# Kernel optimization log

Hardware: AMD Instinct MI355X
Metric: run time of the kernel (lower is better)

## Reference

```python
import jax, jax.numpy as jnp
import numpy as np

DELTA = 6.0      # 3 / (1 - alpha), alpha = 0.5
ETA = 1.0
MS_ITER = 3
D_FEAT = 256
N_PTS = 8192
X_SCALE = 0.06   # keeps ||x||^2 ~ 0.9 so exp(DELTA * X^T X) is well-conditioned


def setup_inputs() -> dict:
    key = jax.random.key(0)
    X = jax.random.normal(key, (D_FEAT, N_PTS), dtype=jnp.float32) * X_SCALE
    return {"X": X}


def _mean_shift_once(X):
    # X: [d, N]
    S = jnp.einsum('dn,dm->nm', X, X)          # X^T X, [N, N]
    K = jnp.exp(DELTA * S)                     # Gaussian-like affinity, [N, N]
    colsum = jnp.sum(K, axis=0)                # d = K^T @ ones  -> column sums, [N]
    # X @ P with P = (1-eta) I + eta K D_inv; D_inv = diag(1/colsum).
    # X @ K @ D_inv == (X @ K) / colsum (per-column scaling) -- no diag/eye materialized.
    XK = X @ K                                 # [d, N]
    return (1.0 - ETA) * X + ETA * (XK / colsum[None, :])


def reference(X):
    outs = []
    cur = X
    for _ in range(MS_ITER):
        cur = _mean_shift_once(cur)
        outs.append(cur)
    return tuple(outs)
```

## Files before the change

### kernel.cpp

```cpp
#include <hip/hip_runtime.h>
#include <hip/hip_bf16.h>
#include <stdint.h>

#define DFEAT 256
#define NPTS  8192

typedef __attribute__((ext_vector_type(8)))  short bf16x8;
typedef __attribute__((ext_vector_type(16))) float f32x16;
typedef __attribute__((ext_vector_type(4)))  int   int4v;
typedef __attribute__((ext_vector_type(4)))  float f32x4;

#define AS1 __attribute__((address_space(1)))
#define AS3 __attribute__((address_space(3)))

__device__ inline void dma16(const void* g, void* l) {
  __builtin_amdgcn_global_load_lds((const AS1 uint32_t*)g, (AS3 uint32_t*)l, 16, 0, 0);
}

__device__ inline uint16_t f2bf(float f) {
  union { float f; uint32_t u; } v; v.f = f;
  return (uint16_t)((v.u + 0x7FFFu + ((v.u >> 16) & 1u)) >> 16);
}


__global__ __launch_bounds__(256, 2) void ms_fused(
    const uint16_t* __restrict__ xaf,
    const uint16_t* __restrict__ xbf,
    float* __restrict__ num,
    float* __restrict__ cs)
{
  __shared__ __attribute__((aligned(16))) uint16_t XT[2][16384];
  __shared__ __attribute__((aligned(16))) uint16_t Ps[2][4096];

  const int tid  = threadIdx.x;
  const int w    = tid >> 6;
  const int lane = tid & 63;
  const int l31  = lane & 31;
  const int g    = lane >> 5;
  const int bid  = blockIdx.x;
  const int mt   = (bid & 1) | ((bid >> 3) << 1);
  const int q    = (bid >> 1) & 3;
  const int m0   = mt * 64;
  const int a_sub = w >> 1;
  const int b_sub = w & 1;

  const char* xafc = (const char*)xaf;
  const char* xbfc = (const char*)xbf;
  char*       XTc  = (char*)XT;
  char*       Psc  = (char*)Ps;

  bf16x8 Bm[16];
  {
    const char* bp = xafc + (size_t)(m0 / 32 + b_sub) * 16384 + g * 512 + l31 * 16;
    #pragma unroll
    for (int ks = 0; ks < 16; ++ks)
      Bm[ks] = __builtin_bit_cast(bf16x8, *(const int4v*)(bp + ks * 1024));
  }

  f32x16 accO[2][2];
  #pragma unroll
  for (int i = 0; i < 2; ++i)
    #pragma unroll
    for (int j = 0; j < 2; ++j)
      #pragma unroll
      for (int r = 0; r < 16; ++r) accO[i][j][r] = 0.0f;
  float csacc = 0.0f;

  const int mloc = 32 * b_sub + l31;
  const int l7   = l31 & 7;
  const int j0   = q * 32;

  {
    const char* src = xafc + (size_t)j0 * 32768;
    #pragma unroll
    for (int r = 0; r < 8; ++r)
      dma16(src + tid * 16 + r * 4096, XTc + tid * 16 + r * 4096);
  }
  __syncthreads();

  bf16x8 XfE[2][4], XfO[2][4];

#define MS_BODY(T_, CUR_, XF_LD, XF_USE, DO_PV)                               \
  {                                                                           \
    const int jt_ = j0 + (T_);                                                \
    char*       psW_ = Psc + (CUR_) * 8192;                                   \
    const char* psR_ = Psc + ((CUR_) ^ 1) * 8192;                             \
                         \
    if ((T_) < 31) {                                                          \
      const char* src_ = xafc + (size_t)(jt_ + 1) * 32768;                    \
      _Pragma("unroll")                                                       \
      for (int r = 0; r < 8; ++r)                                             \
        dma16(src_ + tid * 16 + r * 4096,                                     \
              XTc + ((CUR_) ^ 1) * 32768 + tid * 16 + r * 4096);              \
    }                                                                         \
                                \
    {                                                                         \
      const int n0_ = jt_ * 64;                                               \
      _Pragma("unroll")                                                       \
      for (int t2 = 0; t2 < 2; ++t2) {                                        \
        const char* xp_ = xbfc + (size_t)(2 * w + t2) * 524288 +              \
                          (size_t)(n0_ >> 3) * 512 + g * 512 + l31 * 16;      \
        _Pragma("unroll")                                                     \
        for (int ks = 0; ks < 4; ++ks)                                        \
          XF_LD[t2][ks] =                                                     \
              __builtin_bit_cast(bf16x8, *(const int4v*)(xp_ + ks * 1024));   \
      }                                                                       \
    }                                                                         \
              \
    __builtin_amdgcn_sched_barrier(0x38F);                                    \
              \
    f32x16 s;                                                                 \
    _Pragma("unroll")                                                         \
    for (int r = 0; r < 16; ++r) s[r] = 0.0f;                                 \
    {                                                                         \
      const char* ap_ = XTc + (CUR_) * 32768 + a_sub * 16384 + g * 512 +      \
                        l31 * 16;                                             \
      _Pragma("unroll")                                                       \
      for (int ks = 0; ks < 16; ++ks) {                                       \
        bf16x8 A = __builtin_bit_cast(bf16x8,                                 \
                                      *(const int4v*)(ap_ + ks * 1024));      \
        s = __builtin_amdgcn_mfma_f32_32x32x16_bf16(A, Bm[ks], s, 0, 0, 0);   \
      }                                                                       \
    }                                                                         \
                                \
    if (DO_PV) {                                                              \
      _Pragma("unroll")                                                       \
      for (int ks = 0; ks < 4; ++ks) {                                        \
        bf16x8 Bp[2];                                                         \
        _Pragma("unroll")                                                     \
        for (int mm = 0; mm < 2; ++mm) {                                      \
          int mrow = 32 * mm + l31;                                           \
          int p = (2 * ks + g) ^ l7;                                          \
          Bp[mm] = __builtin_bit_cast(bf16x8,                                 \
              *(const int4v*)(psR_ + mrow * 128 + p * 16));                   \
        }                                                                     \
        _Pragma("unroll")                                                     \
        for (int t2 = 0; t2 < 2; ++t2) {                                      \
          accO[t2][0] = __builtin_amdgcn_mfma_f32_32x32x16_bf16(              \
              XF_USE[t2][ks], Bp[0], accO[t2][0], 0, 0, 0);                   \
          accO[t2][1] = __builtin_amdgcn_mfma_f32_32x32x16_bf16(              \
              XF_USE[t2][ks], Bp[1], accO[t2][1], 0, 0, 0);                   \
        }                                                                     \
      }                                                                       \
    }                                                                         \
                        \
    _Pragma("unroll")                                                         \
    for (int k = 0; k < 4; ++k) {                                             \
      float e0 = __expf(6.0f * s[4 * k + 0]);                                 \
      float e1 = __expf(6.0f * s[4 * k + 1]);                                 \
      float e2 = __expf(6.0f * s[4 * k + 2]);                                 \
      float e3 = __expf(6.0f * s[4 * k + 3]);                                 \
      csacc += (e0 + e1) + (e2 + e3);                                         \
      uint32_t lo, hi;                                                        \
      asm("v_cvt_pk_bf16_f32 %0, %1, %2" : "=v"(lo) : "v"(e0), "v"(e1));      \
      asm("v_cvt_pk_bf16_f32 %0, %1, %2" : "=v"(hi) : "v"(e2), "v"(e3));      \
      int p = (4 * a_sub + k) ^ (mloc & 7);                                   \
      *(uint64_t*)(psW_ + mloc * 128 + p * 16 + 8 * g) =                      \
          ((uint64_t)hi << 32) | lo;                                          \
    }                                                                         \
          \
    asm volatile("s_waitcnt vmcnt(8) lgkmcnt(0)" ::: "memory");               \
    __builtin_amdgcn_s_barrier();                                             \
  }

  MS_BODY(0, 0, XfE, XfO, false)
  for (int tp = 0; tp < 15; ++tp) {
    const int tb = 2 * tp;
    MS_BODY(tb + 1, 1, XfO, XfE, true)
    MS_BODY(tb + 2, 0, XfE, XfO, true)
  }
  MS_BODY(31, 1, XfO, XfE, true)
#undef MS_BODY

  {
    const char* psR = Psc + 8192;
    #pragma unroll
    for (int ks = 0; ks < 4; ++ks) {
      bf16x8 Bp[2];
      #pragma unroll
      for (int mm = 0; mm < 2; ++mm) {
        int mrow = 32 * mm + l31;
        int p = (2 * ks + g) ^ l7;
        Bp[mm] = __builtin_bit_cast(bf16x8,
            *(const int4v*)(psR + mrow * 128 + p * 16));
      }
      #pragma unroll
      for (int t2 = 0; t2 < 2; ++t2) {
        accO[t2][0] = __builtin_amdgcn_mfma_f32_32x32x16_bf16(XfO[t2][ks], Bp[0], accO[t2][0], 0,0,0);
        accO[t2][1] = __builtin_amdgcn_mfma_f32_32x32x16_bf16(XfO[t2][ks], Bp[1], accO[t2][1], 0,0,0);
      }
    }
  }

  csacc += __shfl_xor(csacc, 32, 64);
  if (g == 0) atomicAdd(&cs[m0 + mloc], csacc);
  #pragma unroll
  for (int t2 = 0; t2 < 2; ++t2)
    #pragma unroll
    for (int mm = 0; mm < 2; ++mm)
      #pragma unroll
      for (int r = 0; r < 16; ++r) {
        int drow = 32 * (2 * w + t2) + (r & 3) + 8 * (r >> 2) + 4 * g;
        int mg   = m0 + 32 * mm + l31;
        atomicAdd(&num[(size_t)drow * NPTS + mg], accO[t2][mm][r]);
      }
}

__global__ __launch_bounds__(256) void ms_combine(
    const float* __restrict__ src, const float* __restrict__ csr,
    float* __restrict__ csz, float* __restrict__ yout,
    float* __restrict__ numz,
    uint16_t* __restrict__ xaf, uint16_t* __restrict__ xbf,
    const int mode)
{
  __shared__ uint16_t T[64][66];
  const int tid = threadIdx.x;
  const int n0 = blockIdx.x * 64;
  const int d0 = blockIdx.y * 64;

  #pragma unroll
  for (int i = 0; i < 4; ++i) {
    int e  = tid + i * 256;
    int dl = e >> 4, nq = e & 15;
    size_t idx = (size_t)(d0 + dl) * NPTS + (n0 + nq * 4);
    f32x4 v = *(const f32x4*)(src + idx);
    if (mode) {
      f32x4 c = *(const f32x4*)(csr + n0 + nq * 4);
      v /= c;
      *(f32x4*)(yout + idx) = v;
      f32x4 z = {0.f, 0.f, 0.f, 0.f};
      *(f32x4*)(numz + idx) = z;
    }
    #pragma unroll
    for (int k = 0; k < 4; ++k) T[dl][nq * 4 + k] = f2bf(v[k]);
  }
  if (mode && blockIdx.y == 0 && tid < 64) csz[n0 + tid] = 0.0f;
  __syncthreads();

  char* xafc = (char*)xaf;
  char* xbfc = (char*)xbf;
  #pragma unroll
  for (int i = 0; i < 2; ++i) {
    int c  = tid + i * 256;
    int nb = c >> 8, s2 = (c >> 5) & 7, ln = c & 31;
    union { uint32_t u[4]; int4v v; } pk;
    #pragma unroll
    for (int k = 0; k < 4; ++k) {
      uint32_t lo = T[s2 * 8 + 2 * k][nb * 32 + ln];
      uint32_t hi = T[s2 * 8 + 2 * k + 1][nb * 32 + ln];
      pk.u[k] = lo | (hi << 16);
    }
    *(int4v*)(xafc + (size_t)(n0 / 32 + nb) * 16384 +
              (size_t)(d0 / 8 + s2) * 512 + ln * 16) = pk.v;
  }
  #pragma unroll
  for (int i = 0; i < 2; ++i) {
    int c  = tid + i * 256;
    int db = c >> 8, uu = (c >> 5) & 7, ln = c & 31;
    const uint16_t* tr = &T[db * 32 + ln][uu * 8];
    union { uint32_t u[4]; int4v v; } pk;
    #pragma unroll
    for (int k = 0; k < 4; ++k)
      pk.u[k] = (uint32_t)tr[2 * k] | ((uint32_t)tr[2 * k + 1] << 16);
    *(int4v*)(xbfc + (size_t)(d0 / 32 + db) * 524288 +
              (size_t)(n0 / 8 + uu) * 512 + ln * 16) = pk.v;
  }
}

extern "C" void kernel_launch(void* const* d_in, const int* in_sizes, int n_in,
                              void* d_out, int out_size, void* d_ws, size_t ws_size,
                              hipStream_t stream)
{
  (void)in_sizes; (void)n_in; (void)out_size; (void)ws_size;
  const float* X = (const float*)d_in[0];
  float* out = (float*)d_out;
  char* ws = (char*)d_ws;
  uint16_t* xaf = (uint16_t*)(ws);
  uint16_t* xbf = (uint16_t*)(ws + (4u << 20));
  float*    num = (float*)   (ws + (8u << 20));
  float*    cs0 = (float*)   (ws + (16u << 20));
  float*    cs1 = (float*)   (ws + (16u << 20) + 32768);

  hipMemsetAsync(ws + (8u << 20), 0, (8u << 20) + 65536, stream);

  dim3 cgrid(NPTS / 64, DFEAT / 64);
  ms_combine<<<cgrid, 256, 0, stream>>>(X, nullptr, nullptr, nullptr, nullptr,
                                        xaf, xbf, 0);
  for (int it = 0; it < 3; ++it) {
    float* csA = (it & 1) ? cs1 : cs0;
    float* csB = (it & 1) ? cs0 : cs1;
    ms_fused<<<512, 256, 0, stream>>>(xaf, xbf, num, csA);
    ms_combine<<<cgrid, 256, 0, stream>>>(num, csA, csB,
                                          out + (size_t)it * DFEAT * NPTS,
                                          num, xaf, xbf, 1);
  }
}
```

Measured before the change: 337.5 us.

## Replace global atomic accumulation with per-split partial buffers reduced in combine

Instead of atomically adding partial numerator and column-sum results into shared global buffers, each of the four q-splits writes its own partial slab with plain stores, and the combine kernel sums the four slabs (and eight column-sum partials) before normalizing. This removes the atomic traffic and the memset/zeroing of accumulators. In exchange it costs more workspace and four times the numerator read traffic in the combine kernel.

```diff
diff --git a/kernel.cpp b/kernel.cpp
--- a/kernel.cpp
+++ b/kernel.cpp
@@ -26,8 +26,8 @@
 __global__ __launch_bounds__(256, 2) void ms_fused(
     const uint16_t* __restrict__ xaf,
     const uint16_t* __restrict__ xbf,
-    float* __restrict__ num,
-    float* __restrict__ cs)
+    float* __restrict__ nump,
+    float* __restrict__ csp)
 {
   __shared__ __attribute__((aligned(16))) uint16_t XT[2][16384];
   __shared__ __attribute__((aligned(16))) uint16_t Ps[2][4096];
@@ -193,7 +193,8 @@
   }
 
   csacc += __shfl_xor(csacc, 32, 64);
-  if (g == 0) atomicAdd(&cs[m0 + mloc], csacc);
+  if (g == 0) csp[(size_t)(2 * q + a_sub) * NPTS + m0 + mloc] = csacc;
+  float* np = nump + (size_t)q * (DFEAT * (size_t)NPTS);
   #pragma unroll
   for (int t2 = 0; t2 < 2; ++t2)
     #pragma unroll
@@ -202,14 +203,13 @@
       for (int r = 0; r < 16; ++r) {
         int drow = 32 * (2 * w + t2) + (r & 3) + 8 * (r >> 2) + 4 * g;
         int mg   = m0 + 32 * mm + l31;
-        atomicAdd(&num[(size_t)drow * NPTS + mg], accO[t2][mm][r]);
+        np[(size_t)drow * NPTS + mg] = accO[t2][mm][r];
       }
 }
 
 __global__ __launch_bounds__(256) void ms_combine(
-    const float* __restrict__ src, const float* __restrict__ csr,
-    float* __restrict__ csz, float* __restrict__ yout,
-    float* __restrict__ numz,
+    const float* __restrict__ src, const float* __restrict__ csp,
+    float* __restrict__ yout,
     uint16_t* __restrict__ xaf, uint16_t* __restrict__ xbf,
     const int mode)
 {
@@ -218,6 +218,17 @@
   const int n0 = blockIdx.x * 64;
   const int d0 = blockIdx.y * 64;
 
+  f32x4 rinv;
+  if (mode) {
+    const int nq = tid & 15;
+    f32x4 c = *(const f32x4*)(csp + n0 + nq * 4);
+    #pragma unroll
+    for (int s2 = 1; s2 < 8; ++s2)
+      c += *(const f32x4*)(csp + (size_t)s2 * NPTS + n0 + nq * 4);
+    rinv[0] = 1.0f / c[0]; rinv[1] = 1.0f / c[1];
+    rinv[2] = 1.0f / c[2]; rinv[3] = 1.0f / c[3];
+  }
+
   #pragma unroll
   for (int i = 0; i < 4; ++i) {
     int e  = tid + i * 256;
@@ -225,16 +236,15 @@
     size_t idx = (size_t)(d0 + dl) * NPTS + (n0 + nq * 4);
     f32x4 v = *(const f32x4*)(src + idx);
     if (mode) {
-      f32x4 c = *(const f32x4*)(csr + n0 + nq * 4);
-      v /= c;
+      v += *(const f32x4*)(src + idx + (size_t)1 * DFEAT * NPTS);
+      v += *(const f32x4*)(src + idx + (size_t)2 * DFEAT * NPTS);
+      v += *(const f32x4*)(src + idx + (size_t)3 * DFEAT * NPTS);
+      v *= rinv;
       *(f32x4*)(yout + idx) = v;
-      f32x4 z = {0.f, 0.f, 0.f, 0.f};
-      *(f32x4*)(numz + idx) = z;
     }
     #pragma unroll
     for (int k = 0; k < 4; ++k) T[dl][nq * 4 + k] = f2bf(v[k]);
   }
-  if (mode && blockIdx.y == 0 && tid < 64) csz[n0 + tid] = 0.0f;
   __syncthreads();
 
   char* xafc = (char*)xaf;
@@ -275,23 +285,18 @@
   const float* X = (const float*)d_in[0];
   float* out = (float*)d_out;
   char* ws = (char*)d_ws;
-  uint16_t* xaf = (uint16_t*)(ws);
-  uint16_t* xbf = (uint16_t*)(ws + (4u << 20));
-  float*    num = (float*)   (ws + (8u << 20));
-  float*    cs0 = (float*)   (ws + (16u << 20));
-  float*    cs1 = (float*)   (ws + (16u << 20) + 32768);
-
-  hipMemsetAsync(ws + (8u << 20), 0, (8u << 20) + 65536, stream);
+  uint16_t* xaf  = (uint16_t*)(ws);
+  uint16_t* xbf  = (uint16_t*)(ws + (4u << 20));
+  float*    nump = (float*)   (ws + (8u << 20));
+  float*    csp  = (float*)   (ws + (40u << 20));
+
 
   dim3 cgrid(NPTS / 64, DFEAT / 64);
-  ms_combine<<<cgrid, 256, 0, stream>>>(X, nullptr, nullptr, nullptr, nullptr,
-                                        xaf, xbf, 0);
+  ms_combine<<<cgrid, 256, 0, stream>>>(X, nullptr, nullptr, xaf, xbf, 0);
   for (int it = 0; it < 3; ++it) {
-    float* csA = (it & 1) ? cs1 : cs0;
-    float* csB = (it & 1) ? cs0 : cs1;
-    ms_fused<<<512, 256, 0, stream>>>(xaf, xbf, num, csA);
-    ms_combine<<<cgrid, 256, 0, stream>>>(num, csA, csB,
+    ms_fused<<<512, 256, 0, stream>>>(xaf, xbf, nump, csp);
+    ms_combine<<<cgrid, 256, 0, stream>>>(nump, csp,
                                           out + (size_t)it * DFEAT * NPTS,
-                                          num, xaf, xbf, 1);
-  }
-}
+                                          xaf, xbf, 1);
+  }
+}
```

After: 303.3 us. 1.11x faster.
